# Performance work log

Hardware: AMD Instinct MI355X
Metric: run time of the kernel (lower is better)

The kernel has to match this reference:

```python
import jax, jax.numpy as jnp
import numpy as np

LN_EPS = 1e-5

def setup_inputs() -> dict:
    key = jax.random.key(0)
    k1, k2, k3 = jax.random.split(key, 3)
    L, B, D = 2048, 8, 1024
    x = jax.random.normal(k1, (L, B, D), dtype=jnp.float32)
    c = jnp.zeros((B, D), dtype=jnp.float32)
    W = jax.random.normal(k2, (D, 3 * D), dtype=jnp.float32) * 0.02
    # bias init from _init_bias: u-bias 0, f-bias 0.5, r-bias 0
    b = jnp.concatenate([jnp.zeros(D), jnp.full((D,), 0.5), jnp.zeros(D)]).astype(jnp.float32)
    gamma = jnp.ones((D,), dtype=jnp.float32)
    beta = jnp.zeros((D,), dtype=jnp.float32)
    return {"x": x, "c": c, "W": W, "b": b, "gamma": gamma, "beta": beta}

def reference(x, c, W, b, gamma, beta):
    # LayerNorm over last dim
    mu = jnp.mean(x, axis=-1, keepdims=True)
    var = jnp.mean(jnp.square(x - mu), axis=-1, keepdims=True)
    x_norm = (x - mu) * jax.lax.rsqrt(var + LN_EPS) * gamma + beta
    # Fused u/f/r projection: [L,B,3D]
    ufr = jnp.einsum('lbd,de->lbe', x_norm, W) + b
    u, f, r = jnp.split(ufr, 3, axis=-1)
    f_gate = jax.nn.sigmoid(f)
    r_gate = jax.nn.sigmoid(r)
    # Linear recurrence c_t = f_t * c_{t-1} + (1-f_t) * u_t via scan over time
    def step(c_prev, fu):
        f_t, u_t = fu
        c_t = f_t * c_prev + (1.0 - f_t) * u_t
        return c_t, c_t
    last_c, c_stack = jax.lax.scan(step, c, (f_gate, u))
    hs = r_gate * jnp.tanh(c_stack) + (1.0 - r_gate) * x_norm
    return x + hs, last_c
```

## Files before the change

kernel.cpp:

```cpp
#include <hip/hip_runtime.h>
#include <hip/hip_bf16.h>


typedef unsigned short u16;
typedef __bf16 bf16x8 __attribute__((ext_vector_type(8)));
typedef float f32x4 __attribute__((ext_vector_type(4)));

#define L_DIM 2048
#define B_DIM 8
#define D_DIM 1024
#define M_DIM (L_DIM * B_DIM)
#define K_DIM D_DIM
#define N_DIM (3 * D_DIM)
#define NCH 32
#define CLEN (L_DIM / NCH)
#define NT (K_DIM / 64)

#define LDS_A 0
#define LDS_B 65536
#define LDS_DUMMY 131072
#define LDS_TOTAL 147456

__device__ __forceinline__ float bf2f(u16 h) {
    unsigned int u = ((unsigned int)h) << 16;
    float f;
    __builtin_memcpy(&f, &u, 4);
    return f;
}

__device__ __forceinline__ u16 f2bf(float f) {
    unsigned int u;
    __builtin_memcpy(&u, &f, 4);
    u = u + 0x7fff + ((u >> 16) & 1);
    return (u16)(u >> 16);
}

__device__ __forceinline__ void async16(void* lds, const void* g) {
    __builtin_amdgcn_global_load_lds(
        (const __attribute__((address_space(1))) void*)g,
        (__attribute__((address_space(3))) void*)lds, 16, 0, 0);
}

__global__ __launch_bounds__(256) void ln_kernel(const float* __restrict__ x,
                                                 const float* __restrict__ gamma,
                                                 const float* __restrict__ beta,
                                                 u16* __restrict__ xn,
                                                 float2* __restrict__ mrs) {
    int row = blockIdx.x;
    int tid = threadIdx.x;
    const float4* xr = (const float4*)(x + (size_t)row * D_DIM);
    float4 v = xr[tid];
    float s = v.x + v.y + v.z + v.w;
    float q = v.x * v.x + v.y * v.y + v.z * v.z + v.w * v.w;
    #pragma unroll
    for (int off = 32; off; off >>= 1) {
        s += __shfl_down(s, off);
        q += __shfl_down(q, off);
    }
    __shared__ float ss[4], qq[4];
    int lane = tid & 63, wv = tid >> 6;
    if (lane == 0) { ss[wv] = s; qq[wv] = q; }
    __syncthreads();
    s = ss[0] + ss[1] + ss[2] + ss[3];
    q = qq[0] + qq[1] + qq[2] + qq[3];
    float mu = s * (1.0f / D_DIM);
    float var = q * (1.0f / D_DIM) - mu * mu;
    float rs = rsqrtf(var + 1e-5f);
    if (tid == 0) mrs[row] = make_float2(mu, rs);
    float4 g = ((const float4*)gamma)[tid];
    float4 bt = ((const float4*)beta)[tid];
    ushort4 o;
    o.x = f2bf((v.x - mu) * rs * g.x + bt.x);
    o.y = f2bf((v.y - mu) * rs * g.y + bt.y);
    o.z = f2bf((v.z - mu) * rs * g.z + bt.z);
    o.w = f2bf((v.w - mu) * rs * g.w + bt.w);
    ((ushort4*)(xn + (size_t)row * D_DIM))[tid] = o;
}

__global__ __launch_bounds__(256) void wt_kernel(const float* __restrict__ W,
                                                 u16* __restrict__ Wt) {
    __shared__ float t[64][65];
    int k0 = blockIdx.x * 64;
    int n0 = blockIdx.y * 64;
    int col = threadIdx.x & 63;
    int rg4 = threadIdx.x >> 6;
    #pragma unroll
    for (int j = 0; j < 16; ++j) {
        int r = rg4 * 16 + j;
        t[r][col] = W[(size_t)(k0 + r) * N_DIM + n0 + col];
    }
    __syncthreads();
    #pragma unroll
    for (int j = 0; j < 16; ++j) {
        int nr = rg4 * 16 + j;
        Wt[(size_t)(n0 + nr) * K_DIM + k0 + col] = f2bf(t[col][nr]);
    }
}

__device__ __forceinline__ void stage_half(const u16* __restrict__ gsrc, int base0,
                                           int t, int h, char* lds, int ldsOp,
                                           int tid, int wave) {
    int tc = (t < NT) ? t : 0;
    int k0 = tc * 64;
    char* dst0 = (t < NT) ? (lds + ldsOp + (t & 1) * 32768 + h * 16384)
                          : (lds + LDS_DUMMY);
    #pragma unroll
    for (int s = 0; s < 2; ++s) {
        int c = s * 512 + tid;
        int row = h * 128 + (c >> 3);
        int cc = (c & 7) ^ (row & 7);
        async16(dst0 + s * 8192 + wave * 1024,
                gsrc + (size_t)(base0 + row) * K_DIM + k0 + cc * 8);
    }
}

__global__ __launch_bounds__(512, 2) void gemm_kernel(const u16* __restrict__ A,
                                                      const u16* __restrict__ Bt,
                                                      const float* __restrict__ bias,
                                                      u16* __restrict__ uo,
                                                      u16* __restrict__ fo,
                                                      u16* __restrict__ ro) {
    extern __shared__ char lds[];
    const int tid = threadIdx.x;
    const int wave = tid >> 6, lane = tid & 63;
    const int lm = lane & 15, lg = lane >> 4;
    const int wm = wave >> 2, wn = wave & 3;
    const int bid = blockIdx.x;
    const int wg = (bid & 7) * 96 + (bid >> 3);
    const int m0 = (wg & 63) * 256;
    const int n0 = (wg >> 6) * 256;

    f32x4 acc[8][4] = {};
    bf16x8 av[4][2], aw[4][2], bv[4][2];

#define LDA(dst, bb, mf0)                                                       \
    do { _Pragma("unroll")                                                      \
        for (int q = 0; q < 4; ++q) {                                           \
            int row_ = wm * 128 + ((mf0) + q) * 16 + lm;                        \
            const char* p_ = lds + LDS_A + (bb) * 32768 + row_ * 128;           \
            _Pragma("unroll")                                                   \
            for (int kk = 0; kk < 2; ++kk)                                      \
                dst[q][kk] = *(const bf16x8*)(p_ + ((((kk << 2) | lg) ^ (row_ & 7)) << 4)); \
        } } while (0)

#define LDB(bb, kk)                                                             \
    do { _Pragma("unroll")                                                      \
        for (int nf = 0; nf < 4; ++nf) {                                        \
            int row_ = wn * 64 + nf * 16 + lm;                                  \
            bv[nf][kk] = *(const bf16x8*)(lds + LDS_B + (bb) * 32768 + row_ * 128 \
                                          + ((((kk << 2) | lg) ^ (row_ & 7)) << 4)); \
        } } while (0)

#define MFMA16(r0, afr, kk)                                                     \
    do { _Pragma("unroll")                                                      \
        for (int q = 0; q < 4; ++q)                                             \
            _Pragma("unroll")                                                   \
            for (int nf = 0; nf < 4; ++nf)                                      \
                acc[(r0) + q][nf] = __builtin_amdgcn_mfma_f32_16x16x32_bf16(    \
                    afr[q][kk], bv[nf][kk], acc[(r0) + q][nf], 0, 0, 0);        \
    } while (0)

#define PH_SYNC()                                                               \
    do { __builtin_amdgcn_s_barrier();                                          \
         asm volatile("s_waitcnt lgkmcnt(0)");                                  \
         __builtin_amdgcn_sched_barrier(0); } while (0)

#define TILE_BODY(t, bb, last)                                                  \
    do {                                                                        \
             \
        stage_half(A, m0, (t) + 1, 0, lds, LDS_A, tid, wave);                   \
        LDA(av, bb, 0);                                                         \
        LDB(bb, 0);                                                             \
        PH_SYNC();                                                              \
        __builtin_amdgcn_s_setprio(1);  MFMA16(0, av, 0);                       \
        __builtin_amdgcn_s_setprio(0);  __builtin_amdgcn_s_barrier();           \
                                  \
        stage_half(A, m0, (t) + 1, 1, lds, LDS_A, tid, wave);                   \
        LDB(bb, 1);                                                             \
        PH_SYNC();                                                              \
        __builtin_amdgcn_s_setprio(1);  MFMA16(0, av, 1);                       \
        __builtin_amdgcn_s_setprio(0);  __builtin_amdgcn_s_barrier();           \
                                \
        stage_half(Bt, n0, (t) + 2, 0, lds, LDS_B, tid, wave);                  \
        LDA(aw, bb, 4);                                                         \
        PH_SYNC();                                                              \
        __builtin_amdgcn_s_setprio(1);  MFMA16(4, aw, 0);                       \
        __builtin_amdgcn_s_setprio(0);  __builtin_amdgcn_s_barrier();           \
                                   \
        stage_half(Bt, n0, (t) + 2, 1, lds, LDS_B, tid, wave);                  \
        __builtin_amdgcn_s_barrier();                                           \
        __builtin_amdgcn_s_setprio(1);  MFMA16(4, aw, 1);                       \
        __builtin_amdgcn_s_setprio(0);                                          \
        if (!(last)) asm volatile("s_waitcnt vmcnt(4)" ::: "memory");           \
        __builtin_amdgcn_s_barrier();                                           \
    } while (0)

    stage_half(A, m0, 0, 0, lds, LDS_A, tid, wave);
    stage_half(A, m0, 0, 1, lds, LDS_A, tid, wave);
    stage_half(Bt, n0, 0, 0, lds, LDS_B, tid, wave);
    stage_half(Bt, n0, 0, 1, lds, LDS_B, tid, wave);
    stage_half(Bt, n0, 1, 0, lds, LDS_B, tid, wave);
    stage_half(Bt, n0, 1, 1, lds, LDS_B, tid, wave);
    asm volatile("s_waitcnt vmcnt(4)" ::: "memory");
    __builtin_amdgcn_s_barrier();

    for (int t = 0; t < NT - 2; t += 2) {
        TILE_BODY(t, 0, 0);
        TILE_BODY(t + 1, 1, 0);
    }
    TILE_BODY(NT - 2, 0, 0);
    TILE_BODY(NT - 1, 1, 1);

    int seg = n0 >> 10;
    u16* outp = (seg == 0) ? uo : ((seg == 1) ? fo : ro);
    #pragma unroll
    for (int nf = 0; nf < 4; ++nf) {
        int col = n0 + wn * 64 + nf * 16 + lm;
        int cm = col & 1023;
        float bb2 = bias[col];
        #pragma unroll
        for (int mf = 0; mf < 8; ++mf) {
            #pragma unroll
            for (int j = 0; j < 4; ++j) {
                int row = m0 + wm * 128 + mf * 16 + lg * 4 + j;
                float val = acc[mf][nf][j] + bb2;
                if (seg != 0) val = 1.0f / (1.0f + __expf(-val));
                outp[(size_t)row * D_DIM + cm] = f2bf(val);
            }
        }
    }
#undef LDA
#undef LDB
#undef MFMA16
#undef PH_SYNC
#undef TILE_BODY
}

__global__ __launch_bounds__(256) void scan1_kernel(const u16* __restrict__ fg,
                                                    const u16* __restrict__ u,
                                                    float* __restrict__ Aa,
                                                    float* __restrict__ Ss) {
    int ch = blockIdx.x;
    int bd = (blockIdx.y * 256 + threadIdx.x) * 2;
    int b = bd >> 10, d = bd & 1023;
    float a0 = 1.0f, a1 = 1.0f, s0 = 0.0f, s1 = 0.0f;
    for (int t = ch * CLEN; t < ch * CLEN + CLEN; ++t) {
        size_t idx = ((size_t)(t * B_DIM + b) << 10) + d;
        ushort2 f2 = *(const ushort2*)(fg + idx);
        ushort2 u2 = *(const ushort2*)(u + idx);
        float f0 = bf2f(f2.x), f1 = bf2f(f2.y);
        float v0 = bf2f(u2.x), v1 = bf2f(u2.y);
        s0 = f0 * s0 + (1.0f - f0) * v0;
        s1 = f1 * s1 + (1.0f - f1) * v1;
        a0 *= f0;
        a1 *= f1;
    }
    int o = ch * 8192 + bd;
    *(float2*)(Aa + o) = make_float2(a0, a1);
    *(float2*)(Ss + o) = make_float2(s0, s1);
}

__global__ __launch_bounds__(256) void scan2_kernel(const float* __restrict__ Aa,
                                                    const float* __restrict__ Ss,
                                                    const float* __restrict__ c0,
                                                    float* __restrict__ cs,
                                                    float* __restrict__ lastc) {
    int bd = blockIdx.x * 256 + threadIdx.x;
    float c = c0[bd];
    #pragma unroll 4
    for (int ch = 0; ch < NCH; ++ch) {
        cs[ch * 8192 + bd] = c;
        c = Aa[ch * 8192 + bd] * c + Ss[ch * 8192 + bd];
    }
    lastc[bd] = c;
}

__global__ __launch_bounds__(256) void scan3_kernel(const float* __restrict__ cs,
                                                    const u16* __restrict__ fg,
                                                    const u16* __restrict__ u,
                                                    const u16* __restrict__ rg,
                                                    const float2* __restrict__ mrs,
                                                    const float* __restrict__ gamma,
                                                    const float* __restrict__ beta,
                                                    const float* __restrict__ x,
                                                    float* __restrict__ out) {
    int ch = blockIdx.x;
    int bd = (blockIdx.y * 256 + threadIdx.x) * 2;
    int b = bd >> 10, d = bd & 1023;
    float2 gm = *(const float2*)(gamma + d);
    float2 bt = *(const float2*)(beta + d);
    float c0v = cs[ch * 8192 + bd];
    float c1v = cs[ch * 8192 + bd + 1];
    for (int t = ch * CLEN; t < ch * CLEN + CLEN; ++t) {
        size_t idx = ((size_t)(t * B_DIM + b) << 10) + d;
        ushort2 f2 = *(const ushort2*)(fg + idx);
        ushort2 u2 = *(const ushort2*)(u + idx);
        ushort2 r2 = *(const ushort2*)(rg + idx);
        float2 x2 = *(const float2*)(x + idx);
        float2 mr = mrs[t * B_DIM + b];
        float f0 = bf2f(f2.x), f1 = bf2f(f2.y);
        float v0 = bf2f(u2.x), v1 = bf2f(u2.y);
        float r0 = bf2f(r2.x), r1 = bf2f(r2.y);
        float n0 = (x2.x - mr.x) * mr.y * gm.x + bt.x;
        float n1 = (x2.y - mr.x) * mr.y * gm.y + bt.y;
        c0v = f0 * c0v + (1.0f - f0) * v0;
        c1v = f1 * c1v + (1.0f - f1) * v1;
        float h0 = r0 * tanhf(c0v) + (1.0f - r0) * n0;
        float h1 = r1 * tanhf(c1v) + (1.0f - r1) * n1;
        *(float2*)(out + idx) = make_float2(x2.x + h0, x2.y + h1);
    }
}

extern "C" void kernel_launch(void* const* d_in, const int* in_sizes, int n_in,
                              void* d_out, int out_size, void* d_ws, size_t ws_size,
                              hipStream_t stream) {
    const float* x     = (const float*)d_in[0];
    const float* c0    = (const float*)d_in[1];
    const float* W     = (const float*)d_in[2];
    const float* b     = (const float*)d_in[3];
    const float* gamma = (const float*)d_in[4];
    const float* beta  = (const float*)d_in[5];
    float* out = (float*)d_out;
    float* lastc = out + (size_t)M_DIM * D_DIM;

    char* w = (char*)d_ws;
    u16* xn = (u16*)w;  w += (size_t)M_DIM * D_DIM * 2;
    u16* Wt = (u16*)w;  w += (size_t)N_DIM * K_DIM * 2;
    u16* ug = (u16*)w;  w += (size_t)M_DIM * D_DIM * 2;
    u16* fg = (u16*)w;  w += (size_t)M_DIM * D_DIM * 2;
    u16* rg = (u16*)w;  w += (size_t)M_DIM * D_DIM * 2;
    float* Aa = (float*)w; w += (size_t)NCH * 8192 * 4;
    float* Ss = (float*)w; w += (size_t)NCH * 8192 * 4;
    float* cs = (float*)w; w += (size_t)NCH * 8192 * 4;
    float2* mrs = (float2*)w; w += (size_t)M_DIM * 8;

    hipFuncSetAttribute(reinterpret_cast<const void*>(gemm_kernel),
                        hipFuncAttributeMaxDynamicSharedMemorySize, LDS_TOTAL);

    ln_kernel<<<M_DIM, 256, 0, stream>>>(x, gamma, beta, xn, mrs);
    wt_kernel<<<dim3(K_DIM / 64, N_DIM / 64), 256, 0, stream>>>(W, Wt);
    gemm_kernel<<<768, 512, LDS_TOTAL, stream>>>(xn, Wt, b, ug, fg, rg);
    scan1_kernel<<<dim3(NCH, 16), 256, 0, stream>>>(fg, ug, Aa, Ss);
    scan2_kernel<<<32, 256, 0, stream>>>(Aa, Ss, c0, cs, lastc);
    scan3_kernel<<<dim3(NCH, 16), 256, 0, stream>>>(cs, fg, ug, rg, mrs, gamma, beta, x, out);
}
```

Baseline: 237.2 us.

## Load pre-swizzled MFMA B fragments directly from global, drop B LDS staging

The weight preprocessing kernel now writes W in an MFMA-fragment-ordered bf16 layout, so each wave can load its B operands straight from global/L2 into registers without staging them through LDS. LDS use shrinks to only the A double buffer, the pipeline is simplified to wait on vmcnt(0) each tile, and the XCD-aware block remapping is replaced by a plain 2D grid. This removes LDS traffic and barriers for B but exposes global load latency inside each tile and loses the prefetch depth and L2-locality grid swizzle.

New measurement: 243.1 us. 1.02x slower.

```diff
diff --git a/kernel.cpp b/kernel.cpp
--- a/kernel.cpp
+++ b/kernel.cpp
@@ -16,10 +16,8 @@
 #define CLEN (L_DIM / NCH)
 #define NT (K_DIM / 64)
 
-#define LDS_A 0
-#define LDS_B 65536
-#define LDS_DUMMY 131072
-#define LDS_TOTAL 147456
+#define LDS_DUMMY 65536
+#define LDS_TOTAL 81920
 
 __device__ __forceinline__ float bf2f(u16 h) {
     unsigned int u = ((unsigned int)h) << 16;
@@ -77,45 +75,42 @@
     ((ushort4*)(xn + (size_t)row * D_DIM))[tid] = o;
 }
 
-__global__ __launch_bounds__(256) void wt_kernel(const float* __restrict__ W,
-                                                 u16* __restrict__ Wt) {
-    __shared__ float t[64][65];
-    int k0 = blockIdx.x * 64;
-    int n0 = blockIdx.y * 64;
-    int col = threadIdx.x & 63;
-    int rg4 = threadIdx.x >> 6;
+__global__ __launch_bounds__(256) void wtf_kernel(const float* __restrict__ W,
+                                                  u16* __restrict__ Wf) {
+    int wv = threadIdx.x >> 6, lane = threadIdx.x & 63;
+    int n16 = blockIdx.x * 4 + wv;
+    int k32 = blockIdx.y;
+    int lm = lane & 15, lg = lane >> 4;
+    int col = n16 * 16 + lm;
+    u16 o[8];
     #pragma unroll
-    for (int j = 0; j < 16; ++j) {
-        int r = rg4 * 16 + j;
-        t[r][col] = W[(size_t)(k0 + r) * N_DIM + n0 + col];
-    }
-    __syncthreads();
-    #pragma unroll
-    for (int j = 0; j < 16; ++j) {
-        int nr = rg4 * 16 + j;
-        Wt[(size_t)(n0 + nr) * K_DIM + k0 + col] = f2bf(t[col][nr]);
-    }
-}
-
-__device__ __forceinline__ void stage_half(const u16* __restrict__ gsrc, int base0,
-                                           int t, int h, char* lds, int ldsOp,
-                                           int tid, int wave) {
+    for (int e = 0; e < 8; ++e) {
+        int row = k32 * 32 + lg * 8 + e;
+        o[e] = f2bf(W[(size_t)row * N_DIM + col]);
+    }
+    u16* dst = Wf + (((size_t)n16 * 32 + k32) << 9) + (lane << 3);
+    *(ulonglong2*)dst = *(ulonglong2*)o;
+}
+
+__device__ __forceinline__ void stage_halfA(const u16* __restrict__ A, int m0,
+                                            int t, int h, char* lds,
+                                            int tid, int wave) {
     int tc = (t < NT) ? t : 0;
+    char* dst0 = (t < NT) ? (lds + (t & 1) * 32768 + h * 16384)
+                          : (lds + LDS_DUMMY);
     int k0 = tc * 64;
-    char* dst0 = (t < NT) ? (lds + ldsOp + (t & 1) * 32768 + h * 16384)
-                          : (lds + LDS_DUMMY);
     #pragma unroll
     for (int s = 0; s < 2; ++s) {
         int c = s * 512 + tid;
         int row = h * 128 + (c >> 3);
         int cc = (c & 7) ^ (row & 7);
         async16(dst0 + s * 8192 + wave * 1024,
-                gsrc + (size_t)(base0 + row) * K_DIM + k0 + cc * 8);
+                A + (size_t)(m0 + row) * K_DIM + k0 + cc * 8);
     }
 }
 
 __global__ __launch_bounds__(512, 2) void gemm_kernel(const u16* __restrict__ A,
-                                                      const u16* __restrict__ Bt,
+                                                      const u16* __restrict__ Wf,
                                                       const float* __restrict__ bias,
                                                       u16* __restrict__ uo,
                                                       u16* __restrict__ fo,
@@ -125,39 +120,35 @@
     const int wave = tid >> 6, lane = tid & 63;
     const int lm = lane & 15, lg = lane >> 4;
     const int wm = wave >> 2, wn = wave & 3;
-    const int bid = blockIdx.x;
-    const int wg = (bid & 7) * 96 + (bid >> 3);
-    const int m0 = (wg & 63) * 256;
-    const int n0 = (wg >> 6) * 256;
+    const int m0 = blockIdx.x * 256;
+    const int n0 = blockIdx.y * 256;
+    const int n16w = (n0 >> 4) + wn * 4;
 
     f32x4 acc[8][4] = {};
-    bf16x8 av[4][2], aw[4][2], bv[4][2];
-
-#define LDA(dst, bb, mf0)                                                       \
+    bf16x8 av[4], bv0[4], bv1[4];
+
+#define LDA(bb, mf0, kk)                                                        \
     do { _Pragma("unroll")                                                      \
         for (int q = 0; q < 4; ++q) {                                           \
             int row_ = wm * 128 + ((mf0) + q) * 16 + lm;                        \
-            const char* p_ = lds + LDS_A + (bb) * 32768 + row_ * 128;           \
-            _Pragma("unroll")                                                   \
-            for (int kk = 0; kk < 2; ++kk)                                      \
-                dst[q][kk] = *(const bf16x8*)(p_ + ((((kk << 2) | lg) ^ (row_ & 7)) << 4)); \
+            av[q] = *(const bf16x8*)(lds + (bb) * 32768 + row_ * 128            \
+                     + (((((kk) << 2) | lg) ^ (lm & 7)) << 4));                 \
         } } while (0)
 
-#define LDB(bb, kk)                                                             \
+#define LDBG(dst, t, kk)                                                        \
     do { _Pragma("unroll")                                                      \
-        for (int nf = 0; nf < 4; ++nf) {                                        \
-            int row_ = wn * 64 + nf * 16 + lm;                                  \
-            bv[nf][kk] = *(const bf16x8*)(lds + LDS_B + (bb) * 32768 + row_ * 128 \
-                                          + ((((kk << 2) | lg) ^ (row_ & 7)) << 4)); \
-        } } while (0)
-
-#define MFMA16(r0, afr, kk)                                                     \
+        for (int nf = 0; nf < 4; ++nf)                                          \
+            dst[nf] = *(const bf16x8*)(Wf + ((size_t)((n16w + nf) * 32          \
+                      + (t) * 2 + (kk)) << 9) + (lane << 3));                   \
+    } while (0)
+
+#define MFMA16(r0, bfr)                                                         \
     do { _Pragma("unroll")                                                      \
         for (int q = 0; q < 4; ++q)                                             \
             _Pragma("unroll")                                                   \
             for (int nf = 0; nf < 4; ++nf)                                      \
                 acc[(r0) + q][nf] = __builtin_amdgcn_mfma_f32_16x16x32_bf16(    \
-                    afr[q][kk], bv[nf][kk], acc[(r0) + q][nf], 0, 0, 0);        \
+                    av[q], bfr[nf], acc[(r0) + q][nf], 0, 0, 0);                \
     } while (0)
 
 #define PH_SYNC()                                                               \
@@ -165,51 +156,45 @@
          asm volatile("s_waitcnt lgkmcnt(0)");                                  \
          __builtin_amdgcn_sched_barrier(0); } while (0)
 
-#define TILE_BODY(t, bb, last)                                                  \
+#define TILE_BODY(t, bb)                                                        \
     do {                                                                        \
-             \
-        stage_half(A, m0, (t) + 1, 0, lds, LDS_A, tid, wave);                   \
-        LDA(av, bb, 0);                                                         \
-        LDB(bb, 0);                                                             \
+                                                                   \
+        LDBG(bv0, (t), 0);                                                      \
+        stage_halfA(A, m0, (t) + 1, 0, lds, tid, wave);                         \
+        LDA(bb, 0, 0);                                                          \
         PH_SYNC();                                                              \
-        __builtin_amdgcn_s_setprio(1);  MFMA16(0, av, 0);                       \
+        __builtin_amdgcn_s_setprio(1);  MFMA16(0, bv0);                         \
         __builtin_amdgcn_s_setprio(0);  __builtin_amdgcn_s_barrier();           \
-                                  \
-        stage_half(A, m0, (t) + 1, 1, lds, LDS_A, tid, wave);                   \
-        LDB(bb, 1);                                                             \
+                                                                   \
+        LDBG(bv1, (t), 1);                                                      \
+        stage_halfA(A, m0, (t) + 1, 1, lds, tid, wave);                         \
+        LDA(bb, 0, 1);                                                          \
         PH_SYNC();                                                              \
-        __builtin_amdgcn_s_setprio(1);  MFMA16(0, av, 1);                       \
+        __builtin_amdgcn_s_setprio(1);  MFMA16(0, bv1);                         \
         __builtin_amdgcn_s_setprio(0);  __builtin_amdgcn_s_barrier();           \
-                                \
-        stage_half(Bt, n0, (t) + 2, 0, lds, LDS_B, tid, wave);                  \
-        LDA(aw, bb, 4);                                                         \
+                                                                   \
+        LDA(bb, 4, 0);                                                          \
         PH_SYNC();                                                              \
-        __builtin_amdgcn_s_setprio(1);  MFMA16(4, aw, 0);                       \
+        __builtin_amdgcn_s_setprio(1);  MFMA16(4, bv0);                         \
         __builtin_amdgcn_s_setprio(0);  __builtin_amdgcn_s_barrier();           \
-                                   \
-        stage_half(Bt, n0, (t) + 2, 1, lds, LDS_B, tid, wave);                  \
-        __builtin_amdgcn_s_barrier();                                           \
-        __builtin_amdgcn_s_setprio(1);  MFMA16(4, aw, 1);                       \
+                                                                   \
+        LDA(bb, 4, 1);                                                          \
+        PH_SYNC();                                                              \
+        __builtin_amdgcn_s_setprio(1);  MFMA16(4, bv1);                         \
         __builtin_amdgcn_s_setprio(0);                                          \
-        if (!(last)) asm volatile("s_waitcnt vmcnt(4)" ::: "memory");           \
+        asm volatile("s_waitcnt vmcnt(0)" ::: "memory");                        \
         __builtin_amdgcn_s_barrier();                                           \
     } while (0)
 
-    stage_half(A, m0, 0, 0, lds, LDS_A, tid, wave);
-    stage_half(A, m0, 0, 1, lds, LDS_A, tid, wave);
-    stage_half(Bt, n0, 0, 0, lds, LDS_B, tid, wave);
-    stage_half(Bt, n0, 0, 1, lds, LDS_B, tid, wave);
-    stage_half(Bt, n0, 1, 0, lds, LDS_B, tid, wave);
-    stage_half(Bt, n0, 1, 1, lds, LDS_B, tid, wave);
-    asm volatile("s_waitcnt vmcnt(4)" ::: "memory");
+    stage_halfA(A, m0, 0, 0, lds, tid, wave);
+    stage_halfA(A, m0, 0, 1, lds, tid, wave);
+    asm volatile("s_waitcnt vmcnt(0)" ::: "memory");
     __builtin_amdgcn_s_barrier();
 
-    for (int t = 0; t < NT - 2; t += 2) {
-        TILE_BODY(t, 0, 0);
-        TILE_BODY(t + 1, 1, 0);
-    }
-    TILE_BODY(NT - 2, 0, 0);
-    TILE_BODY(NT - 1, 1, 1);
+    for (int t = 0; t < NT; t += 2) {
+        TILE_BODY(t, 0);
+        TILE_BODY(t + 1, 1);
+    }
 
     int seg = n0 >> 10;
     u16* outp = (seg == 0) ? uo : ((seg == 1) ? fo : ro);
@@ -230,7 +215,7 @@
         }
     }
 #undef LDA
-#undef LDB
+#undef LDBG
 #undef MFMA16
 #undef PH_SYNC
 #undef TILE_BODY
@@ -325,7 +310,7 @@
 
     char* w = (char*)d_ws;
     u16* xn = (u16*)w;  w += (size_t)M_DIM * D_DIM * 2;
-    u16* Wt = (u16*)w;  w += (size_t)N_DIM * K_DIM * 2;
+    u16* Wf = (u16*)w;  w += (size_t)N_DIM * K_DIM * 2;
     u16* ug = (u16*)w;  w += (size_t)M_DIM * D_DIM * 2;
     u16* fg = (u16*)w;  w += (size_t)M_DIM * D_DIM * 2;
     u16* rg = (u16*)w;  w += (size_t)M_DIM * D_DIM * 2;
@@ -338,8 +323,8 @@
                         hipFuncAttributeMaxDynamicSharedMemorySize, LDS_TOTAL);
 
     ln_kernel<<<M_DIM, 256, 0, stream>>>(x, gamma, beta, xn, mrs);
-    wt_kernel<<<dim3(K_DIM / 64, N_DIM / 64), 256, 0, stream>>>(W, Wt);
-    gemm_kernel<<<768, 512, LDS_TOTAL, stream>>>(xn, Wt, b, ug, fg, rg);
+    wtf_kernel<<<dim3(N_DIM / 64, K_DIM / 32), 256, 0, stream>>>(W, Wf);
+    gemm_kernel<<<dim3(M_DIM / 256, N_DIM / 256), 512, LDS_TOTAL, stream>>>(xn, Wf, b, ug, fg, rg);
     scan1_kernel<<<dim3(NCH, 16), 256, 0, stream>>>(fg, ug, Aa, Ss);
     scan2_kernel<<<32, 256, 0, stream>>>(Aa, Ss, c0, cs, lastc);
     scan3_kernel<<<dim3(NCH, 16), 256, 0, stream>>>(cs, fg, ug, rg, mrs, gamma, beta, x, out);
```
